# Optimization experiments

Hardware: AMD Instinct MI355X
Metric: run time of the kernel (lower is better)

## Reference

```python
import jax, jax.numpy as jnp
import numpy as np

SEQ_LEN = 9
HALF = SEQ_LEN // 2  # padding = 4
EPS = 1e-5


def _bn(x, g, b, m, v):
    # BatchNorm1d in eval mode (running stats); dropout disabled (eval).
    return g * (x - m) * jax.lax.rsqrt(v + EPS) + b


def _segment_avgpool(x, segment_key):
    """Per-consecutive-segment AvgPool1d(k=9, stride=1, pad=4, count_include_pad=False).

    x: [B, D] features ordered in time, segment_key: [B] consecutive segment ids.
    Vectorized: windows never cross segment boundaries, so a global prefix sum
    plus per-frame clamped window bounds reproduces the per-segment pooling.
    """
    B, D = x.shape
    idx = jnp.arange(B)
    changed = segment_key[1:] != segment_key[:-1]
    is_start = jnp.concatenate([jnp.array([True]), changed])
    is_end = jnp.concatenate([changed, jnp.array([True])])
    seg_start = jax.lax.cummax(jnp.where(is_start, idx, 0), axis=0)
    seg_end = jax.lax.cummin(jnp.where(is_end, idx, B - 1), axis=0, reverse=True)
    lo = jnp.maximum(idx - HALF, seg_start)
    hi = jnp.minimum(idx + HALF, seg_end)
    csum = jnp.concatenate([jnp.zeros((1, D), x.dtype), jnp.cumsum(x, axis=0)], axis=0)  # [B+1, D]
    sums = csum[hi + 1] - csum[lo]
    counts = (hi - lo + 1).astype(x.dtype)  # count_include_pad=False
    return sums / counts[:, None]


def setup_inputs() -> dict:
    key = jax.random.key(0)
    ks = jax.random.split(key, 16)
    B, F, D3, H = 16384, 2048, 600, 2048
    n_seg = 200
    inp = {
        'img_feat': jax.random.normal(ks[0], (B, F), jnp.float32),
        'segment_key': jnp.sort(jax.random.randint(ks[1], (B,), 0, n_seg, jnp.int32)),
        # to_3d linear
        'W3d': jax.random.normal(ks[2], (D3, F), jnp.float32) * (1.0 / np.sqrt(F)),
        'b3d': jax.random.normal(ks[3], (D3,), jnp.float32) * 0.01,
        # block 1 (bef_pool): Linear(D3->H) + ReLU + BN
        'W1': jax.random.normal(ks[4], (H, D3), jnp.float32) * (1.0 / np.sqrt(D3)),
        'b1': jax.random.normal(ks[5], (H,), jnp.float32) * 0.01,
        'g1': jnp.ones((H,), jnp.float32),
        'be1': jnp.zeros((H,), jnp.float32),
        'm1': jax.random.normal(ks[6], (H,), jnp.float32) * 0.1,
        'v1': jax.random.uniform(ks[7], (H,), jnp.float32, 0.5, 1.5),
        # block 2 (pain head): Linear(H->H) + ReLU + BN
        'W2': jax.random.normal(ks[8], (H, H), jnp.float32) * (1.0 / np.sqrt(H)),
        'b2': jax.random.normal(ks[9], (H,), jnp.float32) * 0.01,
        'g2': jnp.ones((H,), jnp.float32),
        'be2': jnp.zeros((H,), jnp.float32),
        'm2': jax.random.normal(ks[10], (H,), jnp.float32) * 0.1,
        'v2': jax.random.uniform(ks[11], (H,), jnp.float32, 0.5, 1.5),
        # final pain linear H -> 2
        'Wp': jax.random.normal(ks[12], (2, H), jnp.float32) * (1.0 / np.sqrt(H)),
        'bp': jax.random.normal(ks[13], (2,), jnp.float32) * 0.01,
    }
    return inp


def reference(img_feat, segment_key, W3d, b3d, W1, b1, g1, be1, m1, v1,
              W2, b2, g2, be2, m2, v2, Wp, bp):
    latent_3d = img_feat @ W3d.T + b3d                       # [B, D3]
    h = _bn(jax.nn.relu(latent_3d @ W1.T + b1), g1, be1, m1, v1)  # bef_pool, [B, H]
    pooled = _segment_avgpool(h, segment_key)                # ragged windowed avg
    h2 = _bn(jax.nn.relu(pooled @ W2.T + b2), g2, be2, m2, v2)
    output_pain = h2 @ Wp.T + bp                             # [B, 2]
    pain_pred = jax.nn.softmax(output_pain, axis=1)
    return output_pain, pain_pred
```

## Files before the change

### kernel.cpp

```cpp
#include <hip/hip_runtime.h>
#include <hip/hip_bf16.h>
#include <math.h>
#include <stdint.h>

#define DEVI static __device__ __forceinline__

typedef __attribute__((ext_vector_type(8))) short short8;
typedef __attribute__((ext_vector_type(4))) float f32x4;
typedef __attribute__((ext_vector_type(4))) float float4v;
typedef __attribute__((ext_vector_type(4))) unsigned short ushort4v;
typedef __attribute__((ext_vector_type(8))) unsigned short ushort8;

DEVI unsigned short f2bf(float f) {
  unsigned int u = __builtin_bit_cast(unsigned int, f);
  u += 0x7fffu + ((u >> 16) & 1u);
  return (unsigned short)(u >> 16);
}
DEVI float bf2f(unsigned short s) {
  unsigned int u = ((unsigned int)s) << 16;
  return __builtin_bit_cast(float, u);
}

DEVI void gl_lds16(const unsigned short* g, unsigned short* l) {
  __builtin_amdgcn_global_load_lds(
      (const __attribute__((address_space(1))) void*)g,
      (__attribute__((address_space(3))) void*)l, 16, 0, 0);
}

__global__ __launch_bounds__(256) void cast_pad(const float* __restrict__ src,
                                                unsigned short* __restrict__ dst,
                                                int srcR, int srcC, int dstR, int dstC) {
  size_t n4 = (size_t)dstR * (size_t)dstC / 4;
  for (size_t i = (size_t)blockIdx.x * blockDim.x + threadIdx.x; i < n4;
       i += (size_t)gridDim.x * blockDim.x) {
    size_t e = i * 4;
    int r = (int)(e / (size_t)dstC);
    int c = (int)(e % (size_t)dstC);
    float4v v;
    if (r < srcR && c + 3 < srcC) {
      v = *(const float4v*)(src + (size_t)r * srcC + c);
    } else {
#pragma unroll
      for (int j = 0; j < 4; ++j) {
        int cc = c + j;
        v[j] = (r < srcR && cc < srcC) ? src[(size_t)r * srcC + cc] : 0.f;
      }
    }
    ushort4v o;
#pragma unroll
    for (int j = 0; j < 4; ++j) o[j] = f2bf(v[j]);
    *(ushort4v*)(dst + e) = o;
  }
}

template <int EPI>
__global__ __launch_bounds__(256) void gemm_bt(
    const unsigned short* __restrict__ A, const unsigned short* __restrict__ Bt,
    unsigned short* __restrict__ C, int M, int N, int K,
    const float* __restrict__ bias, int biasN,
    const float* __restrict__ g, const float* __restrict__ be,
    const float* __restrict__ mn, const float* __restrict__ vr) {
  __shared__ unsigned short lA[128 * 64];
  __shared__ unsigned short lB[128 * 64];
  const int tid = threadIdx.x;
  const int wid = tid >> 6;
  const int lane = tid & 63;
  const int rowA0 = blockIdx.x * 128;
  const int rowB0 = blockIdx.y * 128;
  const int wr = (wid >> 1) * 64;
  const int wc = (wid & 1) * 64;
  const int frow = lane & 15;
  const int fk8 = (lane >> 4) * 8;

  f32x4 acc[4][4] = {};

  for (int k0 = 0; k0 < K; k0 += 64) {
    __syncthreads();
#pragma unroll
    for (int i = 0; i < 4; ++i) {
      int basechunk = i * 256 + wid * 64;
      int chunk = basechunk + lane;
      int r = chunk >> 3;
      int cc = chunk & 7;
      gl_lds16(A + (size_t)(rowA0 + r) * K + (k0 + cc * 8), lA + basechunk * 8);
      gl_lds16(Bt + (size_t)(rowB0 + r) * K + (k0 + cc * 8), lB + basechunk * 8);
    }
    __syncthreads();
#pragma unroll
    for (int kk = 0; kk < 2; ++kk) {
      short8 af[4], bfr[4];
#pragma unroll
      for (int fm = 0; fm < 4; ++fm)
        af[fm] = *(const short8*)(lA + (wr + fm * 16 + frow) * 64 + kk * 32 + fk8);
#pragma unroll
      for (int fn = 0; fn < 4; ++fn)
        bfr[fn] = *(const short8*)(lB + (wc + fn * 16 + frow) * 64 + kk * 32 + fk8);
#pragma unroll
      for (int fm = 0; fm < 4; ++fm)
#pragma unroll
        for (int fn = 0; fn < 4; ++fn)
          acc[fm][fn] =
              __builtin_amdgcn_mfma_f32_16x16x32_bf16(af[fm], bfr[fn], acc[fm][fn], 0, 0, 0);
    }
  }

  const int rl = (lane >> 4) * 4;
#pragma unroll
  for (int fn = 0; fn < 4; ++fn) {
    int gc = rowB0 + wc + fn * 16 + frow;
    float bb = (gc < biasN) ? bias[gc] : 0.f;
    float gg = 1.f, bbe = 0.f, mm = 0.f, rs = 1.f;
    if (EPI == 1) {
      gg = g[gc];
      bbe = be[gc];
      mm = mn[gc];
      rs = rsqrtf(vr[gc] + 1e-5f);
    }
#pragma unroll
    for (int fm = 0; fm < 4; ++fm) {
      f32x4 v = acc[fm][fn];
#pragma unroll
      for (int r = 0; r < 4; ++r) {
        int gr = rowA0 + wr + fm * 16 + rl + r;
        float x = v[r] + bb;
        if (EPI == 1) {
          x = fmaxf(x, 0.f);
          x = gg * (x - mm) * rs + bbe;
        }
        C[(size_t)gr * N + gc] = f2bf(x);
      }
    }
  }
}

__global__ __launch_bounds__(256) void pool_seg(const unsigned short* __restrict__ h,
                                                const int* __restrict__ key,
                                                unsigned short* __restrict__ pooled,
                                                int B, int D) {
  int row = blockIdx.x;
  int k0 = key[row];
  int down = 0, up = 0;
  while (down < 4 && row - down - 1 >= 0 && key[row - down - 1] == k0) ++down;
  while (up < 4 && row + up + 1 < B && key[row + up + 1] == k0) ++up;
  float inv = 1.f / (float)(down + up + 1);
  int f0 = threadIdx.x * 8;
  float s[8] = {0.f, 0.f, 0.f, 0.f, 0.f, 0.f, 0.f, 0.f};
  for (int dr = -down; dr <= up; ++dr) {
    ushort8 v = *(const ushort8*)(h + (size_t)(row + dr) * D + f0);
#pragma unroll
    for (int j = 0; j < 8; ++j) s[j] += bf2f(v[j]);
  }
  ushort8 o;
#pragma unroll
  for (int j = 0; j < 8; ++j) o[j] = f2bf(s[j] * inv);
  *(ushort8*)(pooled + (size_t)row * D + f0) = o;
}

__global__ __launch_bounds__(256) void final_head(const unsigned short* __restrict__ h2,
                                                  const float* __restrict__ Wp,
                                                  const float* __restrict__ bp,
                                                  float* __restrict__ out, int B, int H) {
  int row = blockIdx.x;
  int f0 = threadIdx.x * 8;
  ushort8 v = *(const ushort8*)(h2 + (size_t)row * H + f0);
  float4v w0a = *(const float4v*)(Wp + f0);
  float4v w0b = *(const float4v*)(Wp + f0 + 4);
  float4v w1a = *(const float4v*)(Wp + H + f0);
  float4v w1b = *(const float4v*)(Wp + H + f0 + 4);
  float a0 = 0.f, a1 = 0.f;
#pragma unroll
  for (int j = 0; j < 4; ++j) {
    float x0 = bf2f(v[j]), x1 = bf2f(v[j + 4]);
    a0 += x0 * w0a[j] + x1 * w0b[j];
    a1 += x0 * w1a[j] + x1 * w1b[j];
  }
#pragma unroll
  for (int off = 32; off > 0; off >>= 1) {
    a0 += __shfl_down(a0, off);
    a1 += __shfl_down(a1, off);
  }
  __shared__ float red[8];
  int wv = threadIdx.x >> 6;
  if ((threadIdx.x & 63) == 0) {
    red[wv] = a0;
    red[4 + wv] = a1;
  }
  __syncthreads();
  if (threadIdx.x == 0) {
    float o0 = red[0] + red[1] + red[2] + red[3] + bp[0];
    float o1 = red[4] + red[5] + red[6] + red[7] + bp[1];
    out[(size_t)row * 2] = o0;
    out[(size_t)row * 2 + 1] = o1;
    float mx = fmaxf(o0, o1);
    float e0 = expf(o0 - mx), e1 = expf(o1 - mx);
    float sden = e0 + e1;
    out[(size_t)B * 2 + (size_t)row * 2] = e0 / sden;
    out[(size_t)B * 2 + (size_t)row * 2 + 1] = e1 / sden;
  }
}

extern "C" void kernel_launch(void* const* d_in, const int* in_sizes, int n_in,
                              void* d_out, int out_size, void* d_ws, size_t ws_size,
                              hipStream_t stream) {
  (void)n_in; (void)out_size; (void)ws_size;
  const float* img = (const float*)d_in[0];
  const int* segkey = (const int*)d_in[1];
  const float* W3d = (const float*)d_in[2];
  const float* b3d = (const float*)d_in[3];
  const float* W1 = (const float*)d_in[4];
  const float* b1 = (const float*)d_in[5];
  const float* g1 = (const float*)d_in[6];
  const float* be1 = (const float*)d_in[7];
  const float* m1 = (const float*)d_in[8];
  const float* v1 = (const float*)d_in[9];
  const float* W2 = (const float*)d_in[10];
  const float* b2 = (const float*)d_in[11];
  const float* g2 = (const float*)d_in[12];
  const float* be2 = (const float*)d_in[13];
  const float* m2 = (const float*)d_in[14];
  const float* v2 = (const float*)d_in[15];
  const float* Wp = (const float*)d_in[16];
  const float* bp = (const float*)d_in[17];

  const int B = in_sizes[1];
  const int F = in_sizes[0] / B;
  const int D3 = in_sizes[3];
  const int H = in_sizes[5];
  const int D3p = ((D3 + 127) / 128) * 128;

  char* ws = (char*)d_ws;
  size_t off = 0;
  auto alloc = [&](size_t bytes) -> void* {
    void* p = (void*)(ws + off);
    off += (bytes + 255) & ~(size_t)255;
    return p;
  };
  unsigned short* imgb = (unsigned short*)alloc((size_t)B * F * 2);
  unsigned short* W3dp = (unsigned short*)alloc((size_t)D3p * F * 2);
  unsigned short* W1p  = (unsigned short*)alloc((size_t)H * D3p * 2);
  unsigned short* W2b  = (unsigned short*)alloc((size_t)H * H * 2);
  unsigned short* lat  = (unsigned short*)alloc((size_t)B * D3p * 2);
  unsigned short* h    = (unsigned short*)alloc((size_t)B * H * 2);
  unsigned short* pooled = (unsigned short*)alloc((size_t)B * H * 2);
  unsigned short* h2 = imgb;

  float* out = (float*)d_out;

  auto gridFor = [](size_t n4) -> int {
    size_t gsz = (n4 + 255) / 256;
    if (gsz > 4096) gsz = 4096;
    return (int)gsz;
  };

  cast_pad<<<gridFor((size_t)B * F / 4), 256, 0, stream>>>(img, imgb, B, F, B, F);
  cast_pad<<<gridFor((size_t)D3p * F / 4), 256, 0, stream>>>(W3d, W3dp, D3, F, D3p, F);
  cast_pad<<<gridFor((size_t)H * D3p / 4), 256, 0, stream>>>(W1, W1p, H, D3, H, D3p);
  cast_pad<<<gridFor((size_t)H * H / 4), 256, 0, stream>>>(W2, W2b, H, H, H, H);

  dim3 blk(256);
  gemm_bt<0><<<dim3(B / 128, D3p / 128), blk, 0, stream>>>(
      imgb, W3dp, lat, B, D3p, F, b3d, D3, nullptr, nullptr, nullptr, nullptr);
  gemm_bt<1><<<dim3(B / 128, H / 128), blk, 0, stream>>>(
      lat, W1p, h, B, H, D3p, b1, H, g1, be1, m1, v1);
  pool_seg<<<B, H / 8, 0, stream>>>(h, segkey, pooled, B, H);
  gemm_bt<1><<<dim3(B / 128, H / 128), blk, 0, stream>>>(
      pooled, W2b, h2, B, H, H, b2, H, g2, be2, m2, v2);
  final_head<<<B, H / 8, 0, stream>>>(h2, Wp, bp, out, B, H);
}
```

Before: 725.5 us.

## Replace GEMM with 256x256 eight-wave double-buffered swizzled LDS kernel

Replaces the 128x128, 4-wave GEMM with a 256x256, 8-wave kernel that uses 128KB of dynamic LDS with double buffering. Global-to-LDS loads for the next K tile are interleaved between MFMA quadrants. LDS addresses are XOR-swizzled to avoid bank conflicts, and MFMA bursts are bracketed with setprio. The goal is more reuse per tile, latency hiding and fewer LDS conflicts. The trade-offs are that D3 is padded to 768 (more wasted work in the first two GEMMs) and hardcoded, and the larger tiles leave fewer blocks to fill the CUs.

```diff
diff --git a/kernel.cpp b/kernel.cpp
--- a/kernel.cpp
+++ b/kernel.cpp
@@ -53,61 +53,135 @@
   }
 }
 
+#define BARRIER()                                   \
+  do {                                              \
+    asm volatile("" ::: "memory");                  \
+    __builtin_amdgcn_s_barrier();                   \
+    asm volatile("" ::: "memory");                  \
+  } while (0)
+#define LGKM0_SCHED()                                        \
+  do {                                                       \
+    asm volatile("s_waitcnt lgkmcnt(0)" ::: "memory");       \
+    __builtin_amdgcn_sched_barrier(0);                       \
+  } while (0)
+
+#define DSA(fmBase)                                                           \
+  _Pragma("unroll") for (int i_ = 0; i_ < 4; ++i_)                            \
+  _Pragma("unroll") for (int kk_ = 0; kk_ < 2; ++kk_)                         \
+      afr[i_][kk_] = *(const short8*)(ldsc + curOff +                         \
+          ((arow0 + ((fmBase) + i_) * 2048 + kk_ * 64 + fk16) ^ xorv));
+
+#define DSB(fnBase)                                                           \
+  _Pragma("unroll") for (int j_ = 0; j_ < 2; ++j_)                            \
+  _Pragma("unroll") for (int kk_ = 0; kk_ < 2; ++kk_)                         \
+      bfr[j_][kk_] = *(const short8*)(ldsc + 65536 + curOff +                 \
+          ((brow0 + ((fnBase) + j_) * 2048 + kk_ * 64 + fk16) ^ xorv));
+
+#define MFMAQ(fmB, fnB)                                                       \
+  __builtin_amdgcn_s_setprio(1);                                              \
+  _Pragma("unroll") for (int i_ = 0; i_ < 4; ++i_)                            \
+  _Pragma("unroll") for (int j_ = 0; j_ < 2; ++j_)                            \
+  _Pragma("unroll") for (int kk_ = 0; kk_ < 2; ++kk_)                         \
+      acc[(fmB) + i_][(fnB) + j_] = __builtin_amdgcn_mfma_f32_16x16x32_bf16(  \
+          afr[i_][kk_], bfr[j_][kk_], acc[(fmB) + i_][(fnB) + j_], 0, 0, 0);  \
+  __builtin_amdgcn_s_setprio(0);                                              \
+  __builtin_amdgcn_sched_barrier(0);
+
 template <int EPI>
-__global__ __launch_bounds__(256) void gemm_bt(
+__global__ __launch_bounds__(512, 1) void gemm8p(
     const unsigned short* __restrict__ A, const unsigned short* __restrict__ Bt,
     unsigned short* __restrict__ C, int M, int N, int K,
     const float* __restrict__ bias, int biasN,
     const float* __restrict__ g, const float* __restrict__ be,
     const float* __restrict__ mn, const float* __restrict__ vr) {
-  __shared__ unsigned short lA[128 * 64];
-  __shared__ unsigned short lB[128 * 64];
+  extern __shared__ unsigned short lds[];
+  char* ldsc = (char*)lds;
   const int tid = threadIdx.x;
   const int wid = tid >> 6;
   const int lane = tid & 63;
-  const int rowA0 = blockIdx.x * 128;
-  const int rowB0 = blockIdx.y * 128;
-  const int wr = (wid >> 1) * 64;
-  const int wc = (wid & 1) * 64;
+  const int wave_m = wid >> 2;
+  const int wave_n = wid & 3;
+  const int rowA0 = blockIdx.x * 256;
+  const int rowB0 = blockIdx.y * 256;
   const int frow = lane & 15;
-  const int fk8 = (lane >> 4) * 8;
-
-  f32x4 acc[4][4] = {};
-
-  for (int k0 = 0; k0 < K; k0 += 64) {
-    __syncthreads();
-#pragma unroll
-    for (int i = 0; i < 4; ++i) {
-      int basechunk = i * 256 + wid * 64;
-      int chunk = basechunk + lane;
-      int r = chunk >> 3;
-      int cc = chunk & 7;
-      gl_lds16(A + (size_t)(rowA0 + r) * K + (k0 + cc * 8), lA + basechunk * 8);
-      gl_lds16(Bt + (size_t)(rowB0 + r) * K + (k0 + cc * 8), lB + basechunk * 8);
-    }
-    __syncthreads();
-#pragma unroll
-    for (int kk = 0; kk < 2; ++kk) {
-      short8 af[4], bfr[4];
-#pragma unroll
-      for (int fm = 0; fm < 4; ++fm)
-        af[fm] = *(const short8*)(lA + (wr + fm * 16 + frow) * 64 + kk * 32 + fk8);
-#pragma unroll
-      for (int fn = 0; fn < 4; ++fn)
-        bfr[fn] = *(const short8*)(lB + (wc + fn * 16 + frow) * 64 + kk * 32 + fk8);
-#pragma unroll
-      for (int fm = 0; fm < 4; ++fm)
-#pragma unroll
-        for (int fn = 0; fn < 4; ++fn)
-          acc[fm][fn] =
-              __builtin_amdgcn_mfma_f32_16x16x32_bf16(af[fm], bfr[fn], acc[fm][fn], 0, 0, 0);
-    }
+  const int fk16 = (lane >> 4) * 16;
+  const int xorv = (frow & 7) << 4;
+  const int arow0 = (wave_m * 128 + frow) * 128;
+  const int brow0 = (wave_n * 64 + frow) * 128;
+  const int NT = K >> 6;
+
+  f32x4 acc[8][4] = {};
+  short8 afr[4][2], bfr[2][2];
+
+  auto stage = [&](const unsigned short* __restrict__ G, int matBase, int buf, int h,
+                   int tileR0, int k0) {
+#pragma unroll
+    for (int j = 0; j < 2; ++j) {
+      int x = (j * 512 + tid) * 16;
+      int sx = x ^ (((x >> 7) & 7) << 4);
+      int grow = tileR0 + h * 128 + (x >> 7);
+      int gcol = k0 + ((sx & 127) >> 1);
+      unsigned short* lp = (unsigned short*)(ldsc + matBase + buf * 32768 + h * 16384 +
+                                             (j * 8 + wid) * 1024);
+      gl_lds16(G + (size_t)grow * K + gcol, lp);
+    }
+  };
+
+  stage(A, 0, 0, 0, rowA0, 0);
+  stage(A, 0, 0, 1, rowA0, 0);
+  stage(Bt, 65536, 0, 0, rowB0, 0);
+  stage(Bt, 65536, 0, 1, rowB0, 0);
+  if (NT > 1) {
+    stage(A, 0, 1, 0, rowA0, 64);
+    stage(A, 0, 1, 1, rowA0, 64);
+    asm volatile("s_waitcnt vmcnt(4)" ::: "memory");
+  } else {
+    asm volatile("s_waitcnt vmcnt(0)" ::: "memory");
+  }
+  BARRIER();
+
+  for (int t = 0; t < NT; ++t) {
+    const int cur = t & 1;
+    const int curOff = cur * 32768;
+    const int nxt = cur ^ 1;
+    const int k1 = (t + 1) * 64;
+    const int k2 = (t + 2) * 64;
+    DSA(0);
+    DSB(0);
+    if (t + 1 < NT) stage(Bt, 65536, nxt, 0, rowB0, k1);
+    BARRIER();
+    LGKM0_SCHED();
+    MFMAQ(0, 0);
+    BARRIER();
+    DSB(2);
+    if (t + 1 < NT) stage(Bt, 65536, nxt, 1, rowB0, k1);
+    BARRIER();
+    LGKM0_SCHED();
+    MFMAQ(0, 2);
+    BARRIER();
+    DSA(4);
+    BARRIER();
+    LGKM0_SCHED();
+    MFMAQ(4, 2);
+    BARRIER();
+    DSB(0);
+    BARRIER();
+    if (t + 2 < NT) {
+      stage(A, 0, cur, 0, rowA0, k2);
+      stage(A, 0, cur, 1, rowA0, k2);
+      asm volatile("s_waitcnt vmcnt(4)" ::: "memory");
+    } else {
+      asm volatile("s_waitcnt vmcnt(0)" ::: "memory");
+    }
+    LGKM0_SCHED();
+    MFMAQ(4, 0);
+    BARRIER();
   }
 
   const int rl = (lane >> 4) * 4;
 #pragma unroll
   for (int fn = 0; fn < 4; ++fn) {
-    int gc = rowB0 + wc + fn * 16 + frow;
+    int gc = rowB0 + wave_n * 64 + fn * 16 + frow;
     float bb = (gc < biasN) ? bias[gc] : 0.f;
     float gg = 1.f, bbe = 0.f, mm = 0.f, rs = 1.f;
     if (EPI == 1) {
@@ -117,11 +191,11 @@
       rs = rsqrtf(vr[gc] + 1e-5f);
     }
 #pragma unroll
-    for (int fm = 0; fm < 4; ++fm) {
+    for (int fm = 0; fm < 8; ++fm) {
       f32x4 v = acc[fm][fn];
 #pragma unroll
       for (int r = 0; r < 4; ++r) {
-        int gr = rowA0 + wr + fm * 16 + rl + r;
+        int gr = rowA0 + wave_m * 128 + fm * 16 + rl + r;
         float x = v[r] + bb;
         if (EPI == 1) {
           x = fmaxf(x, 0.f);
@@ -226,7 +300,7 @@
   const int F = in_sizes[0] / B;
   const int D3 = in_sizes[3];
   const int H = in_sizes[5];
-  const int D3p = ((D3 + 127) / 128) * 128;
+  const int D3p = 768;
 
   char* ws = (char*)d_ws;
   size_t off = 0;
@@ -252,18 +326,23 @@
     return (int)gsz;
   };
 
+  hipFuncSetAttribute(reinterpret_cast<const void*>(gemm8p<0>),
+                      hipFuncAttributeMaxDynamicSharedMemorySize, 131072);
+  hipFuncSetAttribute(reinterpret_cast<const void*>(gemm8p<1>),
+                      hipFuncAttributeMaxDynamicSharedMemorySize, 131072);
+
   cast_pad<<<gridFor((size_t)B * F / 4), 256, 0, stream>>>(img, imgb, B, F, B, F);
   cast_pad<<<gridFor((size_t)D3p * F / 4), 256, 0, stream>>>(W3d, W3dp, D3, F, D3p, F);
   cast_pad<<<gridFor((size_t)H * D3p / 4), 256, 0, stream>>>(W1, W1p, H, D3, H, D3p);
   cast_pad<<<gridFor((size_t)H * H / 4), 256, 0, stream>>>(W2, W2b, H, H, H, H);
 
-  dim3 blk(256);
-  gemm_bt<0><<<dim3(B / 128, D3p / 128), blk, 0, stream>>>(
+  dim3 blk(512);
+  gemm8p<0><<<dim3(B / 256, D3p / 256), blk, 131072, stream>>>(
       imgb, W3dp, lat, B, D3p, F, b3d, D3, nullptr, nullptr, nullptr, nullptr);
-  gemm_bt<1><<<dim3(B / 128, H / 128), blk, 0, stream>>>(
+  gemm8p<1><<<dim3(B / 256, H / 256), blk, 131072, stream>>>(
       lat, W1p, h, B, H, D3p, b1, H, g1, be1, m1, v1);
   pool_seg<<<B, H / 8, 0, stream>>>(h, segkey, pooled, B, H);
-  gemm_bt<1><<<dim3(B / 128, H / 128), blk, 0, stream>>>(
+  gemm8p<1><<<dim3(B / 256, H / 256), blk, 131072, stream>>>(
       pooled, W2b, h2, B, H, H, b2, H, g2, be2, m2, v2);
   final_head<<<B, H / 8, 0, stream>>>(h2, Wp, bp, out, B, H);
 }
```

Measured after the change: 642.3 us. 11.5% less time.
